# Optimization experiments

Measured on AMD Instinct MI355X. Metric: run time of the kernel, lower is better.

The kernel has to match this reference:

```python
import jax, jax.numpy as jnp
import numpy as np

B, I, H = 64, 1024, 1024

def _linear_params(key, fan_in, fan_out):
    kw, kb = jax.random.split(key)
    bound = 1.0 / np.sqrt(fan_in)
    W = jax.random.uniform(kw, (fan_in, fan_out), minval=-bound, maxval=bound, dtype=jnp.float32)
    b = jax.random.uniform(kb, (fan_out,), minval=-bound, maxval=bound, dtype=jnp.float32)
    return W, b

def setup_inputs() -> dict:
    key = jax.random.key(0)
    ks = jax.random.split(key, 12)
    Wi, bi = _linear_params(ks[0], I + H, H)
    Wf, bf = _linear_params(ks[1], I + H, H)
    Wo, bo = _linear_params(ks[2], I + H, H)
    Wk, bk = _linear_params(ks[3], I, H)
    Wv, bv = _linear_params(ks[4], I, H)
    Wq, bq = _linear_params(ks[5], H, H)
    We, be = _linear_params(ks[6], H, H)
    x = jax.random.normal(ks[7], (B, I), dtype=jnp.float32)
    h_prev = jax.random.normal(ks[8], (B, H), dtype=jnp.float32)
    C_prev = jax.random.normal(ks[9], (B, H, H), dtype=jnp.float32)
    n_prev = jnp.ones((B, H), dtype=jnp.float32)
    return {"x": x, "h_prev": h_prev, "C_prev": C_prev, "n_prev": n_prev,
            "Wi": Wi, "bi": bi, "Wf": Wf, "bf": bf, "Wo": Wo, "bo": bo,
            "Wk": Wk, "bk": bk, "Wv": Wv, "bv": bv, "Wq": Wq, "bq": bq,
            "We": We, "be": be}

def reference(x, h_prev, C_prev, n_prev, Wi, bi, Wf, bf, Wo, bo, Wk, bk, Wv, bv, Wq, bq, We, be):
    combined = jnp.concatenate([x, h_prev], axis=1)            # [B, I+H]
    i_t = jax.nn.sigmoid(combined @ Wi + bi)                   # [B, H]
    f_t = jax.nn.sigmoid(combined @ Wf + bf)
    o_t = jax.nn.sigmoid(combined @ Wo + bo)
    k_t = x @ Wk + bk                                          # [B, H]
    v_t = x @ Wv + bv
    q_t = h_prev @ Wq + bq
    # outer-product memory update: C_t[b] = f*C_prev[b] + i*(v_t[b] ⊗ k_t[b])
    C_t = f_t[:, :, None] * C_prev + i_t[:, :, None] * jnp.einsum('bi,bj->bij', v_t, k_t)
    n_t = f_t * n_prev + i_t * jnp.exp(k_t @ We + be)
    h_t = o_t * (jnp.einsum('bij,bj->bi', C_t, q_t) / n_t)
    return (h_t, C_t, n_t)
```

## Files before the change

kernel.cpp:

```cpp
#include <hip/hip_runtime.h>
#include <math.h>

#define Bn 64
#define Hn 1024
#define BH 65536

typedef float v4f __attribute__((ext_vector_type(4)));

#define WS_GP (6 * BH)
#define WS_NP (54 * BH)

__global__ __launch_bounds__(256) void gates_partial(
    const float* __restrict__ x, const float* __restrict__ h_prev,
    const float* __restrict__ Wi, const float* __restrict__ Wf,
    const float* __restrict__ Wo, const float* __restrict__ Wk,
    const float* __restrict__ Wv, const float* __restrict__ Wq,
    float* __restrict__ ws)
{
    const int g = blockIdx.z, s = blockIdx.y;
    const float* Wm;
    int Ktot;
    switch (g) {
        case 0: Wm = Wi; Ktot = 2048; break;
        case 1: Wm = Wf; Ktot = 2048; break;
        case 2: Wm = Wo; Ktot = 2048; break;
        case 3: Wm = Wk; Ktot = 1024; break;
        case 4: Wm = Wv; Ktot = 1024; break;
        default: Wm = Wq; Ktot = 1024; break;
    }
    const int chunk = Ktot >> 3;
    const int kbase = s * chunk;

    __shared__ float A_lds[64][68];

    const int t  = threadIdx.x;
    const int cg = t & 15;
    const int rg = t >> 4;
    const int n0 = (blockIdx.x << 6) + (cg << 2);

    float4 acc[4];
    #pragma unroll
    for (int r = 0; r < 4; ++r) acc[r] = make_float4(0.f, 0.f, 0.f, 0.f);

    for (int kc = 0; kc < chunk; kc += 64) {
        const int k0 = kbase + kc;
        const float* Ab;
        int kloc;
        if (g < 3)       { Ab = (k0 < 1024) ? x : h_prev; kloc = k0 & 1023; }
        else if (g == 5) { Ab = h_prev; kloc = k0; }
        else             { Ab = x;      kloc = k0; }

        __syncthreads();
        {
            const int c = cg << 2;
            #pragma unroll
            for (int rr = 0; rr < 4; ++rr) {
                const int row = rg + (rr << 4);
                *(float4*)&A_lds[row][c] =
                    *(const float4*)&Ab[(size_t)row * 1024 + kloc + c];
            }
        }
        __syncthreads();

        #pragma unroll 2
        for (int kk = 0; kk < 64; kk += 4) {
            const float* wp = Wm + (size_t)(k0 + kk) * 1024 + n0;
            const float4 w0 = *(const float4*)(wp);
            const float4 w1 = *(const float4*)(wp + 1024);
            const float4 w2 = *(const float4*)(wp + 2048);
            const float4 w3 = *(const float4*)(wp + 3072);
            #pragma unroll
            for (int r = 0; r < 4; ++r) {
                const float4 a = *(const float4*)&A_lds[(rg << 2) + r][kk];
                acc[r].x += a.x * w0.x + a.y * w1.x + a.z * w2.x + a.w * w3.x;
                acc[r].y += a.x * w0.y + a.y * w1.y + a.z * w2.y + a.w * w3.y;
                acc[r].z += a.x * w0.z + a.y * w1.z + a.z * w2.z + a.w * w3.z;
                acc[r].w += a.x * w0.w + a.y * w1.w + a.z * w2.w + a.w * w3.w;
            }
        }
    }

    float* P = ws + WS_GP + (size_t)(g * 8 + s) * BH;
    #pragma unroll
    for (int r = 0; r < 4; ++r)
        *(float4*)&P[(size_t)((rg << 2) + r) * 1024 + n0] = acc[r];
}

__global__ __launch_bounds__(256) void gates_finalize(
    const float* __restrict__ bi, const float* __restrict__ bf,
    const float* __restrict__ bo, const float* __restrict__ bk,
    const float* __restrict__ bv, const float* __restrict__ bq,
    float* __restrict__ ws)
{
    const int v4 = blockIdx.x * 256 + threadIdx.x;
    const int g  = v4 >> 14;
    const int r4 = v4 & 16383;
    const float4* P = (const float4*)(ws + WS_GP + (size_t)g * 8 * BH);
    float4 a = P[r4];
    #pragma unroll
    for (int s = 1; s < 8; ++s) {
        const float4 p = P[(size_t)s * (BH / 4) + r4];
        a.x += p.x; a.y += p.y; a.z += p.z; a.w += p.w;
    }
    const float* bias;
    switch (g) {
        case 0: bias = bi; break; case 1: bias = bf; break;
        case 2: bias = bo; break; case 3: bias = bk; break;
        case 4: bias = bv; break; default: bias = bq; break;
    }
    const float4 b4 = ((const float4*)bias)[r4 & 255];
    a.x += b4.x; a.y += b4.y; a.z += b4.z; a.w += b4.w;
    if (g < 3) {
        a.x = 1.f / (1.f + expf(-a.x));
        a.y = 1.f / (1.f + expf(-a.y));
        a.z = 1.f / (1.f + expf(-a.z));
        a.w = 1.f / (1.f + expf(-a.w));
    }
    ((float4*)ws)[v4] = a;
}

__global__ __launch_bounds__(256) void ngate_partial(
    const float* __restrict__ We, float* __restrict__ ws)
{
    const int s  = blockIdx.y;
    const int k0 = s * 64;
    const float* kt = ws + 3 * BH;

    __shared__ float A_lds[64][68];

    const int t  = threadIdx.x;
    const int cg = t & 15;
    const int rg = t >> 4;
    const int n0 = (blockIdx.x << 6) + (cg << 2);

    float4 acc[4];
    #pragma unroll
    for (int r = 0; r < 4; ++r) acc[r] = make_float4(0.f, 0.f, 0.f, 0.f);

    {
        const int c = cg << 2;
        #pragma unroll
        for (int rr = 0; rr < 4; ++rr) {
            const int row = rg + (rr << 4);
            *(float4*)&A_lds[row][c] =
                *(const float4*)&kt[(size_t)row * 1024 + k0 + c];
        }
    }
    __syncthreads();

    #pragma unroll 2
    for (int kk = 0; kk < 64; kk += 4) {
        const float* wp = We + (size_t)(k0 + kk) * 1024 + n0;
        const float4 w0 = *(const float4*)(wp);
        const float4 w1 = *(const float4*)(wp + 1024);
        const float4 w2 = *(const float4*)(wp + 2048);
        const float4 w3 = *(const float4*)(wp + 3072);
        #pragma unroll
        for (int r = 0; r < 4; ++r) {
            const float4 a = *(const float4*)&A_lds[(rg << 2) + r][kk];
            acc[r].x += a.x * w0.x + a.y * w1.x + a.z * w2.x + a.w * w3.x;
            acc[r].y += a.x * w0.y + a.y * w1.y + a.z * w2.y + a.w * w3.y;
            acc[r].z += a.x * w0.z + a.y * w1.z + a.z * w2.z + a.w * w3.z;
            acc[r].w += a.x * w0.w + a.y * w1.w + a.z * w2.w + a.w * w3.w;
        }
    }

    float* P = ws + WS_NP + (size_t)s * BH;
    #pragma unroll
    for (int r = 0; r < 4; ++r)
        *(float4*)&P[(size_t)((rg << 2) + r) * 1024 + n0] = acc[r];
}

__global__ __launch_bounds__(256) void c_update(
    const float* __restrict__ C_prev, const float* __restrict__ ws,
    const float* __restrict__ be, const float* __restrict__ n_prev,
    float* __restrict__ h_t, float* __restrict__ C_t,
    float* __restrict__ n_out)
{
    const int t    = threadIdx.x;
    const int lane = t & 63;
    const int w    = t >> 6;
    const int R0   = blockIdx.x * 32 + w * 8;
    const int b    = R0 >> 10;

    const float4* kp = (const float4*)(ws + 3 * BH + (size_t)b * 1024);
    const float4* qp = (const float4*)(ws + 5 * BH + (size_t)b * 1024);
    float4 k4[4], q4[4];
    #pragma unroll
    for (int c = 0; c < 4; ++c) {
        k4[c] = kp[c * 64 + lane];
        q4[c] = qp[c * 64 + lane];
    }

    #pragma unroll 2
    for (int r = 0; r < 8; ++r) {
        const int R    = R0 + r;
        const float f  = ws[1 * BH + R];
        const float i_ = ws[0 * BH + R];
        const float iv = i_ * ws[4 * BH + R];

        float m = be[R & 1023];
        #pragma unroll
        for (int s = 0; s < 16; ++s) m += ws[WS_NP + (size_t)s * BH + R];
        const float n = f * n_prev[R] + i_ * expf(m);

        const v4f* cp = (const v4f*)(C_prev + (size_t)R * 1024);
        v4f*       co = (v4f*)(C_t + (size_t)R * 1024);

        float dot = 0.f;
        #pragma unroll
        for (int c = 0; c < 4; ++c) {
            const v4f c4 = __builtin_nontemporal_load(&cp[c * 64 + lane]);
            v4f o4;
            o4.x = f * c4.x + iv * k4[c].x;
            o4.y = f * c4.y + iv * k4[c].y;
            o4.z = f * c4.z + iv * k4[c].z;
            o4.w = f * c4.w + iv * k4[c].w;
            __builtin_nontemporal_store(o4, &co[c * 64 + lane]);
            dot += o4.x * q4[c].x + o4.y * q4[c].y
                 + o4.z * q4[c].z + o4.w * q4[c].w;
        }
        #pragma unroll
        for (int off = 32; off; off >>= 1)
            dot += __shfl_xor(dot, off);
        if (lane == 0) {
            h_t[R]   = ws[2 * BH + R] * dot / n;
            n_out[R] = n;
        }
    }
}

extern "C" void kernel_launch(void* const* d_in, const int* in_sizes, int n_in,
                              void* d_out, int out_size, void* d_ws, size_t ws_size,
                              hipStream_t stream)
{
    const float* x      = (const float*)d_in[0];
    const float* h_prev = (const float*)d_in[1];
    const float* C_prev = (const float*)d_in[2];
    const float* n_prev = (const float*)d_in[3];
    const float* Wi = (const float*)d_in[4];  const float* bi = (const float*)d_in[5];
    const float* Wf = (const float*)d_in[6];  const float* bf = (const float*)d_in[7];
    const float* Wo = (const float*)d_in[8];  const float* bo = (const float*)d_in[9];
    const float* Wk = (const float*)d_in[10]; const float* bk = (const float*)d_in[11];
    const float* Wv = (const float*)d_in[12]; const float* bv = (const float*)d_in[13];
    const float* Wq = (const float*)d_in[14]; const float* bq = (const float*)d_in[15];
    const float* We = (const float*)d_in[16]; const float* be = (const float*)d_in[17];

    float* out = (float*)d_out;
    float* h_t = out;
    float* C_t = out + BH;
    float* n_t = out + BH + (size_t)Bn * Hn * Hn;
    float* ws  = (float*)d_ws;

    gates_partial<<<dim3(16, 8, 6), 256, 0, stream>>>(
        x, h_prev, Wi, Wf, Wo, Wk, Wv, Wq, ws);

    gates_finalize<<<384, 256, 0, stream>>>(
        bi, bf, bo, bk, bv, bq, ws);

    ngate_partial<<<dim3(16, 16), 256, 0, stream>>>(We, ws);

    c_update<<<2048, 256, 0, stream>>>(
        C_prev, ws, be, n_prev, h_t, C_t, n_t);
}
```

Baseline: 521.5 us.

## Eliminate gates_finalize by fusing split-K reductions into consumers, finer split-K

```diff
diff --git a/kernel.cpp b/kernel.cpp
--- a/kernel.cpp
+++ b/kernel.cpp
@@ -8,7 +8,14 @@
 typedef float v4f __attribute__((ext_vector_type(4)));
 
 #define WS_GP (6 * BH)
-#define WS_NP (54 * BH)
+#define NSLOT 144
+#define SLOT_I 0
+#define SLOT_F 32
+#define SLOT_O 64
+#define SLOT_K 96
+#define SLOT_V 112
+#define SLOT_Q 128
+#define WS_NP (WS_GP + NSLOT * BH)
 
 __global__ __launch_bounds__(256) void gates_partial(
     const float* __restrict__ x, const float* __restrict__ h_prev,
@@ -17,19 +24,23 @@
     const float* __restrict__ Wv, const float* __restrict__ Wq,
     float* __restrict__ ws)
 {
-    const int g = blockIdx.z, s = blockIdx.y;
+    const int ys = blockIdx.y;
+    int g, s;
+    if (ys < 96) { g = ys >> 5; s = ys & 31; }
+    else         { const int t2 = ys - 96; g = 3 + (t2 >> 4); s = t2 & 15; }
+
     const float* Wm;
-    int Ktot;
     switch (g) {
-        case 0: Wm = Wi; Ktot = 2048; break;
-        case 1: Wm = Wf; Ktot = 2048; break;
-        case 2: Wm = Wo; Ktot = 2048; break;
-        case 3: Wm = Wk; Ktot = 1024; break;
-        case 4: Wm = Wv; Ktot = 1024; break;
-        default: Wm = Wq; Ktot = 1024; break;
-    }
-    const int chunk = Ktot >> 3;
-    const int kbase = s * chunk;
+        case 0: Wm = Wi; break; case 1: Wm = Wf; break;
+        case 2: Wm = Wo; break; case 3: Wm = Wk; break;
+        case 4: Wm = Wv; break; default: Wm = Wq; break;
+    }
+    const int k0 = s << 6;
+    const float* Ab;
+    int kloc;
+    if (g < 3)       { Ab = (k0 < 1024) ? x : h_prev; kloc = k0 & 1023; }
+    else if (g == 5) { Ab = h_prev; kloc = k0; }
+    else             { Ab = x;      kloc = k0; }
 
     __shared__ float A_lds[64][68];
 
@@ -38,115 +49,82 @@
     const int rg = t >> 4;
     const int n0 = (blockIdx.x << 6) + (cg << 2);
 
+    {
+        const int c = cg << 2;
+        #pragma unroll
+        for (int rr = 0; rr < 4; ++rr) {
+            const int row = rg + (rr << 4);
+            *(float4*)&A_lds[row][c] =
+                *(const float4*)&Ab[(size_t)row * 1024 + kloc + c];
+        }
+    }
+    __syncthreads();
+
     float4 acc[4];
     #pragma unroll
     for (int r = 0; r < 4; ++r) acc[r] = make_float4(0.f, 0.f, 0.f, 0.f);
 
-    for (int kc = 0; kc < chunk; kc += 64) {
-        const int k0 = kbase + kc;
-        const float* Ab;
-        int kloc;
-        if (g < 3)       { Ab = (k0 < 1024) ? x : h_prev; kloc = k0 & 1023; }
-        else if (g == 5) { Ab = h_prev; kloc = k0; }
-        else             { Ab = x;      kloc = k0; }
-
-        __syncthreads();
-        {
-            const int c = cg << 2;
-            #pragma unroll
-            for (int rr = 0; rr < 4; ++rr) {
-                const int row = rg + (rr << 4);
-                *(float4*)&A_lds[row][c] =
-                    *(const float4*)&Ab[(size_t)row * 1024 + kloc + c];
-            }
-        }
-        __syncthreads();
-
-        #pragma unroll 2
-        for (int kk = 0; kk < 64; kk += 4) {
-            const float* wp = Wm + (size_t)(k0 + kk) * 1024 + n0;
-            const float4 w0 = *(const float4*)(wp);
-            const float4 w1 = *(const float4*)(wp + 1024);
-            const float4 w2 = *(const float4*)(wp + 2048);
-            const float4 w3 = *(const float4*)(wp + 3072);
-            #pragma unroll
-            for (int r = 0; r < 4; ++r) {
-                const float4 a = *(const float4*)&A_lds[(rg << 2) + r][kk];
-                acc[r].x += a.x * w0.x + a.y * w1.x + a.z * w2.x + a.w * w3.x;
-                acc[r].y += a.x * w0.y + a.y * w1.y + a.z * w2.y + a.w * w3.y;
-                acc[r].z += a.x * w0.z + a.y * w1.z + a.z * w2.z + a.w * w3.z;
-                acc[r].w += a.x * w0.w + a.y * w1.w + a.z * w2.w + a.w * w3.w;
-            }
-        }
-    }
-
-    float* P = ws + WS_GP + (size_t)(g * 8 + s) * BH;
+    #pragma unroll 2
+    for (int kk = 0; kk < 64; kk += 4) {
+        const float* wp = Wm + (size_t)(k0 + kk) * 1024 + n0;
+        const float4 w0 = *(const float4*)(wp);
+        const float4 w1 = *(const float4*)(wp + 1024);
+        const float4 w2 = *(const float4*)(wp + 2048);
+        const float4 w3 = *(const float4*)(wp + 3072);
+        #pragma unroll
+        for (int r = 0; r < 4; ++r) {
+            const float4 a = *(const float4*)&A_lds[(rg << 2) + r][kk];
+            acc[r].x += a.x * w0.x + a.y * w1.x + a.z * w2.x + a.w * w3.x;
+            acc[r].y += a.x * w0.y + a.y * w1.y + a.z * w2.y + a.w * w3.y;
+            acc[r].z += a.x * w0.z + a.y * w1.z + a.z * w2.z + a.w * w3.z;
+            acc[r].w += a.x * w0.w + a.y * w1.w + a.z * w2.w + a.w * w3.w;
+        }
+    }
+
+    float* P = ws + WS_GP + (size_t)ys * BH;
     #pragma unroll
     for (int r = 0; r < 4; ++r)
         *(float4*)&P[(size_t)((rg << 2) + r) * 1024 + n0] = acc[r];
 }
 
-__global__ __launch_bounds__(256) void gates_finalize(
-    const float* __restrict__ bi, const float* __restrict__ bf,
-    const float* __restrict__ bo, const float* __restrict__ bk,
-    const float* __restrict__ bv, const float* __restrict__ bq,
+__global__ __launch_bounds__(256) void ngate_partial(
+    const float* __restrict__ We, const float* __restrict__ bk,
     float* __restrict__ ws)
 {
-    const int v4 = blockIdx.x * 256 + threadIdx.x;
-    const int g  = v4 >> 14;
-    const int r4 = v4 & 16383;
-    const float4* P = (const float4*)(ws + WS_GP + (size_t)g * 8 * BH);
-    float4 a = P[r4];
-    #pragma unroll
-    for (int s = 1; s < 8; ++s) {
-        const float4 p = P[(size_t)s * (BH / 4) + r4];
-        a.x += p.x; a.y += p.y; a.z += p.z; a.w += p.w;
-    }
-    const float* bias;
-    switch (g) {
-        case 0: bias = bi; break; case 1: bias = bf; break;
-        case 2: bias = bo; break; case 3: bias = bk; break;
-        case 4: bias = bv; break; default: bias = bq; break;
-    }
-    const float4 b4 = ((const float4*)bias)[r4 & 255];
-    a.x += b4.x; a.y += b4.y; a.z += b4.z; a.w += b4.w;
-    if (g < 3) {
-        a.x = 1.f / (1.f + expf(-a.x));
-        a.y = 1.f / (1.f + expf(-a.y));
-        a.z = 1.f / (1.f + expf(-a.z));
-        a.w = 1.f / (1.f + expf(-a.w));
-    }
-    ((float4*)ws)[v4] = a;
-}
-
-__global__ __launch_bounds__(256) void ngate_partial(
-    const float* __restrict__ We, float* __restrict__ ws)
-{
     const int s  = blockIdx.y;
-    const int k0 = s * 64;
-    const float* kt = ws + 3 * BH;
+    const int nx = blockIdx.x;
+    const int k0 = s << 6;
 
     __shared__ float A_lds[64][68];
 
     const int t  = threadIdx.x;
     const int cg = t & 15;
     const int rg = t >> 4;
-    const int n0 = (blockIdx.x << 6) + (cg << 2);
-
-    float4 acc[4];
-    #pragma unroll
-    for (int r = 0; r < 4; ++r) acc[r] = make_float4(0.f, 0.f, 0.f, 0.f);
+    const int n0 = (nx << 6) + (cg << 2);
+    const int c  = cg << 2;
 
     {
-        const int c = cg << 2;
+        const float4 kb = *(const float4*)&bk[k0 + c];
         #pragma unroll
         for (int rr = 0; rr < 4; ++rr) {
             const int row = rg + (rr << 4);
-            *(float4*)&A_lds[row][c] =
-                *(const float4*)&kt[(size_t)row * 1024 + k0 + c];
+            float4 a = kb;
+            #pragma unroll
+            for (int ss = 0; ss < 16; ++ss) {
+                const float4 p = *(const float4*)&ws[WS_GP
+                    + (size_t)(SLOT_K + ss) * BH + (size_t)row * 1024 + k0 + c];
+                a.x += p.x; a.y += p.y; a.z += p.z; a.w += p.w;
+            }
+            *(float4*)&A_lds[row][c] = a;
+            if (nx == 0)
+                *(float4*)&ws[(size_t)3 * BH + (size_t)row * 1024 + k0 + c] = a;
         }
     }
     __syncthreads();
+
+    float4 acc[4];
+    #pragma unroll
+    for (int r = 0; r < 4; ++r) acc[r] = make_float4(0.f, 0.f, 0.f, 0.f);
 
     #pragma unroll 2
     for (int kk = 0; kk < 64; kk += 4) {
@@ -173,36 +151,77 @@
 
 __global__ __launch_bounds__(256) void c_update(
     const float* __restrict__ C_prev, const float* __restrict__ ws,
-    const float* __restrict__ be, const float* __restrict__ n_prev,
+    const float* __restrict__ bi, const float* __restrict__ bf,
+    const float* __restrict__ bo, const float* __restrict__ bv,
+    const float* __restrict__ bq, const float* __restrict__ be,
+    const float* __restrict__ n_prev,
     float* __restrict__ h_t, float* __restrict__ C_t,
     float* __restrict__ n_out)
 {
+    __shared__ float q_f[1024];
+    __shared__ float fs[64], ivs[64], on[64];
+
     const int t    = threadIdx.x;
+    const int orig = blockIdx.x;
+    const int swz  = ((orig & 7) << 7) + (orig >> 3);
+    const int R0   = swz << 6;
+    const int b    = R0 >> 10;
+
+    {
+        float4 a = *(const float4*)&bq[t << 2];
+        const float* base = ws + WS_GP + (size_t)SLOT_Q * BH
+                          + (size_t)b * 1024 + (t << 2);
+        #pragma unroll
+        for (int ss = 0; ss < 16; ++ss) {
+            const float4 p = *(const float4*)(base + (size_t)ss * BH);
+            a.x += p.x; a.y += p.y; a.z += p.z; a.w += p.w;
+        }
+        *(float4*)&q_f[t << 2] = a;
+    }
+
+    if (t < 64) {
+        const int R = R0 + t;
+        const int n = R & 1023;
+        float iv = bi[n], fv = bf[n], ov = bo[n], vv = bv[n], mv = be[n];
+        const float* G = ws + WS_GP;
+        #pragma unroll 4
+        for (int ss = 0; ss < 32; ++ss) iv += G[(size_t)(SLOT_I + ss) * BH + R];
+        #pragma unroll 4
+        for (int ss = 0; ss < 32; ++ss) fv += G[(size_t)(SLOT_F + ss) * BH + R];
+        #pragma unroll 4
+        for (int ss = 0; ss < 32; ++ss) ov += G[(size_t)(SLOT_O + ss) * BH + R];
+        #pragma unroll 4
+        for (int ss = 0; ss < 16; ++ss) vv += G[(size_t)(SLOT_V + ss) * BH + R];
+        #pragma unroll 4
+        for (int ss = 0; ss < 16; ++ss) mv += ws[WS_NP + (size_t)ss * BH + R];
+        const float ig = 1.f / (1.f + expf(-iv));
+        const float fg = 1.f / (1.f + expf(-fv));
+        const float og = 1.f / (1.f + expf(-ov));
+        const float nt = fg * n_prev[R] + ig * expf(mv);
+        n_out[R] = nt;
+        fs[t]  = fg;
+        ivs[t] = ig * vv;
+        on[t]  = og / nt;
+    }
+    __syncthreads();
+
     const int lane = t & 63;
     const int w    = t >> 6;
-    const int R0   = blockIdx.x * 32 + w * 8;
-    const int b    = R0 >> 10;
-
+
+    float4 k4[4], q4[4];
     const float4* kp = (const float4*)(ws + 3 * BH + (size_t)b * 1024);
-    const float4* qp = (const float4*)(ws + 5 * BH + (size_t)b * 1024);
-    float4 k4[4], q4[4];
     #pragma unroll
     for (int c = 0; c < 4; ++c) {
         k4[c] = kp[c * 64 + lane];
-        q4[c] = qp[c * 64 + lane];
+        q4[c] = *(const float4*)&q_f[(c * 64 + lane) << 2];
     }
 
     #pragma unroll 2
-    for (int r = 0; r < 8; ++r) {
-        const int R    = R0 + r;
-        const float f  = ws[1 * BH + R];
-        const float i_ = ws[0 * BH + R];
-        const float iv = i_ * ws[4 * BH + R];
-
-        float m = be[R & 1023];
-        #pragma unroll
-        for (int s = 0; s < 16; ++s) m += ws[WS_NP + (size_t)s * BH + R];
-        const float n = f * n_prev[R] + i_ * expf(m);
+    for (int r = 0; r < 16; ++r) {
+        const int lr = (w << 4) + r;
+        const int R  = R0 + lr;
+        const float f  = fs[lr];
+        const float iv = ivs[lr];
 
         const v4f* cp = (const v4f*)(C_prev + (size_t)R * 1024);
         v4f*       co = (v4f*)(C_t + (size_t)R * 1024);
@@ -223,10 +242,8 @@
         #pragma unroll
         for (int off = 32; off; off >>= 1)
             dot += __shfl_xor(dot, off);
-        if (lane == 0) {
-            h_t[R]   = ws[2 * BH + R] * dot / n;
-            n_out[R] = n;
-        }
+        if (lane == 0)
+            h_t[R] = on[lr] * dot;
     }
 }
 
@@ -252,14 +269,11 @@
     float* n_t = out + BH + (size_t)Bn * Hn * Hn;
     float* ws  = (float*)d_ws;
 
-    gates_partial<<<dim3(16, 8, 6), 256, 0, stream>>>(
+    gates_partial<<<dim3(16, 144), 256, 0, stream>>>(
         x, h_prev, Wi, Wf, Wo, Wk, Wv, Wq, ws);
 
-    gates_finalize<<<384, 256, 0, stream>>>(
-        bi, bf, bo, bk, bv, bq, ws);
-
-    ngate_partial<<<dim3(16, 16), 256, 0, stream>>>(We, ws);
-
-    c_update<<<2048, 256, 0, stream>>>(
-        C_prev, ws, be, n_prev, h_t, C_t, n_t);
-}
+    ngate_partial<<<dim3(16, 16), 256, 0, stream>>>(We, bk, ws);
+
+    c_update<<<1024, 256, 0, stream>>>(
+        C_prev, ws, bi, bf, bo, bv, bq, be, n_prev, h_t, C_t, n_t);
+}
```

After: 543.4 us. +4.2%, slower.
